# Kernel tuning notes

Measured on AMD Instinct MI355X. Metric: run time of the kernel, lower is better.

The kernel has to match this reference:

```python
import jax, jax.numpy as jnp
import numpy as np

K = 131072
C = 128
THR = 9.2885e-30


def setup_inputs() -> dict:
    key = jax.random.key(0)
    k1, k2, k3, k4, k5 = jax.random.split(key, 5)
    scores1 = jax.random.normal(k1, (K, C), dtype=jnp.float32)
    scores2 = jax.random.normal(k2, (K, C), dtype=jnp.float32)
    # Build lineages hitting the three supported branches, never the
    # unsupported overlapping-but-unequal case (which raises in torch).
    c1 = jax.random.randint(k3, (K,), 0, C)
    off = jax.random.randint(k4, (K,), 1, C)
    c2 = (c1 + off) % C  # guaranteed != c1
    case = jax.random.randint(k5, (K,), 0, 3)  # 0: equal 1-hot, 1: equal 2-hot, 2: disjoint 1-hots
    oh1 = jax.nn.one_hot(c1, C, dtype=jnp.int32)
    oh2 = jax.nn.one_hot(c2, C, dtype=jnp.int32)
    is1 = (case == 1)[:, None]
    is2 = (case == 2)[:, None]
    Y1 = oh1 + jnp.where(is1, oh2, 0)
    Y2 = jnp.where(is2, oh2, Y1)
    return {"scores1": scores1, "Y1": Y1, "scores2": scores2, "Y2": Y2}


def reference(scores1, Y1, scores2, Y2):
    P1 = jax.nn.softmax(scores1, axis=1)  # [K, C]
    P2 = jax.nn.softmax(scores2, axis=1)
    L1 = Y1.astype(P1.dtype)
    L2 = Y2.astype(P2.dtype)

    eq = jnp.all(Y1 == Y2, axis=1)
    s = jnp.sum(Y1, axis=1)
    case1 = eq & (s == 1)   # equal one-hot lineage
    case2 = eq & (s == 2)   # equal two-hot lineage

    nclass = scores1.shape[1]
    rows = jnp.arange(scores1.shape[0])
    idx_a = jnp.argmax(Y1, axis=1)                      # first nonzero
    idx_b = nclass - 1 - jnp.argmax(Y1[:, ::-1], axis=1)  # last nonzero
    p1a = P1[rows, idx_a]; p1b = P1[rows, idx_b]
    p2a = P2[rows, idx_a]; p2b = P2[rows, idx_b]

    def safe_neglog(p):
        return jnp.where(p > THR, -jnp.log(jnp.maximum(p, THR)), 0.0)

    # case1: -log P1[i,c] - log P2[i,c] (each term thresholded)
    loss1 = safe_neglog(p1a) + safe_neglog(p2a)

    # case2: split two-hot into l1 (first pos), l2 (second pos); both one-hot
    # so disjunction == gathered prob.
    prob2 = 1.0 - (1.0 - p1a * p2b) * (1.0 - p1b * p2a)
    loss2 = safe_neglog(prob2)

    # default disjoint case: vectorized disjunction D(l,p) = 1 - prod(1 - l*p)
    D11 = 1.0 - jnp.prod(1.0 - L1 * P1, axis=1)  # Px1_Y1
    D21 = 1.0 - jnp.prod(1.0 - L2 * P1, axis=1)  # Px1_Y2
    D12 = 1.0 - jnp.prod(1.0 - L1 * P2, axis=1)  # Px2_Y1
    D22 = 1.0 - jnp.prod(1.0 - L2 * P2, axis=1)  # Px2_Y2
    probd = 1.0 - (1.0 - D11 * D22) * (1.0 - D21 * D12)
    lossd = safe_neglog(probd)

    return jnp.where(case1, loss1, jnp.where(case2, loss2, lossd))
```

## Files before the change

### kernel.cpp

```cpp
#include <hip/hip_runtime.h>


constexpr int KROWS = 131072;
constexpr int CC    = 128;
#define THRF 9.2885e-30f

typedef float  f32x4 __attribute__((ext_vector_type(4)));
typedef int    i32x4 __attribute__((ext_vector_type(4)));
typedef float  f32x2 __attribute__((ext_vector_type(2)));

__device__ __forceinline__ float hredsumf(float v){
#pragma unroll
  for (int m = 16; m > 0; m >>= 1) v += __shfl_xor(v, m, 32);
  return v;
}

__device__ __forceinline__ float sel4(float p0, float p1, float p2, float p3, int s){
  float lo = (s & 1) ? p1 : p0;
  float hi = (s & 1) ? p3 : p2;
  return (s & 2) ? hi : lo;
}

__device__ __forceinline__ float gatherP(float p0, float p1, float p2, float p3, int idx){
  float c = sel4(p0, p1, p2, p3, idx & 3);
  return __shfl(c, (idx >> 2) & 31, 32);
}

__device__ __forceinline__ float computeRow(
    f32x4 a1, f32x4 a2, i32x4 b1, i32x4 b2, bool hi)
{
  float e10 = __expf(a1.x), e11 = __expf(a1.y), e12 = __expf(a1.z), e13 = __expf(a1.w);
  float e20 = __expf(a2.x), e21 = __expf(a2.y), e22 = __expf(a2.z), e23 = __expf(a2.w);
  float inv1 = 1.0f / hredsumf(e10 + e11 + e12 + e13);
  float inv2 = 1.0f / hredsumf(e20 + e21 + e22 + e23);

  unsigned long long M0 = __ballot((b1.x | b2.x) != 0);
  unsigned long long M1 = __ballot((b1.y | b2.y) != 0);
  unsigned long long M2 = __ballot((b1.z | b2.z) != 0);
  unsigned long long M3 = __ballot((b1.w | b2.w) != 0);

  unsigned int h[4];
  h[0] = hi ? (unsigned int)(M0 >> 32) : (unsigned int)M0;
  h[1] = hi ? (unsigned int)(M1 >> 32) : (unsigned int)M1;
  h[2] = hi ? (unsigned int)(M2 >> 32) : (unsigned int)M2;
  h[3] = hi ? (unsigned int)(M3 >> 32) : (unsigned int)M3;

  int u = 1 << 30, v = -1;
#pragma unroll
  for (int j = 0; j < 4; ++j) {
    if (h[j]) {
      u = min(u, ((__ffs(h[j]) - 1) << 2) + j);
      v = max(v, ((31 - __clz(h[j])) << 2) + j);
    }
  }

  float p1u = gatherP(e10, e11, e12, e13, u) * inv1;
  float p1v = gatherP(e10, e11, e12, e13, v) * inv1;
  float p2u = gatherP(e20, e21, e22, e23, u) * inv2;
  float p2v = gatherP(e20, e21, e22, e23, v) * inv2;

  float x = p1u * p2v;
  float y = p1v * p2u;
  float prob = (u == v) ? x : 1.0f - (1.0f - x) * (1.0f - y);
  return (prob > THRF) ? -__logf(prob) : 0.0f;
}

__global__ __launch_bounds__(256) void wmc_loss_kernel(
    const float* __restrict__ s1, const int* __restrict__ y1,
    const float* __restrict__ s2, const int* __restrict__ y2,
    float* __restrict__ out)
{
  const int hw   = threadIdx.x >> 5;
  const int lane = threadIdx.x & 31;
  const bool hi  = (threadIdx.x & 32) != 0;
  const int row0 = blockIdx.x * 16 + hw * 2;

  const size_t base0 = (size_t)row0 * CC;
  const size_t base1 = base0 + CC;

  const f32x4 A10 = __builtin_nontemporal_load(((const f32x4*)(s1 + base0)) + lane);
  const f32x4 A20 = __builtin_nontemporal_load(((const f32x4*)(s2 + base0)) + lane);
  const i32x4 B10 = __builtin_nontemporal_load(((const i32x4*)(y1 + base0)) + lane);
  const i32x4 B20 = __builtin_nontemporal_load(((const i32x4*)(y2 + base0)) + lane);
  const f32x4 A11 = __builtin_nontemporal_load(((const f32x4*)(s1 + base1)) + lane);
  const f32x4 A21 = __builtin_nontemporal_load(((const f32x4*)(s2 + base1)) + lane);
  const i32x4 B11 = __builtin_nontemporal_load(((const i32x4*)(y1 + base1)) + lane);
  const i32x4 B21 = __builtin_nontemporal_load(((const i32x4*)(y2 + base1)) + lane);

  float l0 = computeRow(A10, A20, B10, B20, hi);
  float l1 = computeRow(A11, A21, B11, B21, hi);

  if (lane == 0) {
    f32x2 o; o.x = l0; o.y = l1;
    __builtin_nontemporal_store(o, (f32x2*)(out + row0));
  }
}

extern "C" void kernel_launch(void* const* d_in, const int* in_sizes, int n_in,
                              void* d_out, int out_size, void* d_ws, size_t ws_size,
                              hipStream_t stream) {
  const float* s1 = (const float*)d_in[0];
  const int*   y1 = (const int*)d_in[1];
  const float* s2 = (const float*)d_in[2];
  const int*   y2 = (const int*)d_in[3];
  float* out = (float*)d_out;

  dim3 grid(KROWS / 16), block(256);
  wmc_loss_kernel<<<grid, block, 0, stream>>>(s1, y1, s2, y2, out);
}
```

Before: 210.1 us.

## Use persistent grid-stride blocks with software-prefetched row pairs

The launch shrinks from one block per 16 rows to 2048 blocks that each loop over 4 row groups. Inside the loop the next iteration's row pair is loaded before the current one is computed. The goal is to overlap global-memory latency with the softmax and gather work and to cut block launch overhead. In exchange each wave holds more live registers for the double-buffered loads, and there are fewer waves in flight to hide latency.

```diff
diff --git a/kernel.cpp b/kernel.cpp
--- a/kernel.cpp
+++ b/kernel.cpp
@@ -1,8 +1,12 @@
 #include <hip/hip_runtime.h>
 
 
-constexpr int KROWS = 131072;
-constexpr int CC    = 128;
+constexpr int KROWS   = 131072;
+constexpr int CC      = 128;
+constexpr int NBLOCKS = 2048;
+constexpr int RPB     = 16;
+constexpr int NITER   = KROWS / (NBLOCKS * RPB);
+constexpr int STRIDE  = NBLOCKS * RPB;
 #define THRF 9.2885e-30f
 
 typedef float  f32x4 __attribute__((ext_vector_type(4)));
@@ -65,6 +69,40 @@
   return (prob > THRF) ? -__logf(prob) : 0.0f;
 }
 
+struct RowPair {
+  f32x4 a10, a20, a11, a21;
+  i32x4 b10, b20, b11, b21;
+};
+
+__device__ __forceinline__ RowPair loadPair(
+    const float* s1, const int* y1, const float* s2, const int* y2,
+    int row0, int lane)
+{
+  RowPair t;
+  const size_t base0 = (size_t)row0 * CC;
+  const size_t base1 = base0 + CC;
+  t.a10 = __builtin_nontemporal_load(((const f32x4*)(s1 + base0)) + lane);
+  t.a20 = __builtin_nontemporal_load(((const f32x4*)(s2 + base0)) + lane);
+  t.b10 = __builtin_nontemporal_load(((const i32x4*)(y1 + base0)) + lane);
+  t.b20 = __builtin_nontemporal_load(((const i32x4*)(y2 + base0)) + lane);
+  t.a11 = __builtin_nontemporal_load(((const f32x4*)(s1 + base1)) + lane);
+  t.a21 = __builtin_nontemporal_load(((const f32x4*)(s2 + base1)) + lane);
+  t.b11 = __builtin_nontemporal_load(((const i32x4*)(y1 + base1)) + lane);
+  t.b21 = __builtin_nontemporal_load(((const i32x4*)(y2 + base1)) + lane);
+  return t;
+}
+
+__device__ __forceinline__ void computeStore(
+    const RowPair& P, bool hi, int lane, int row, float* out)
+{
+  float l0 = computeRow(P.a10, P.a20, P.b10, P.b20, hi);
+  float l1 = computeRow(P.a11, P.a21, P.b11, P.b21, hi);
+  if (lane == 0) {
+    f32x2 o; o.x = l0; o.y = l1;
+    __builtin_nontemporal_store(o, (f32x2*)(out + row));
+  }
+}
+
 __global__ __launch_bounds__(256) void wmc_loss_kernel(
     const float* __restrict__ s1, const int* __restrict__ y1,
     const float* __restrict__ s2, const int* __restrict__ y2,
@@ -73,26 +111,18 @@
   const int hw   = threadIdx.x >> 5;
   const int lane = threadIdx.x & 31;
   const bool hi  = (threadIdx.x & 32) != 0;
-  const int row0 = blockIdx.x * 16 + hw * 2;
+  int row = blockIdx.x * RPB + hw * 2;
 
-  const size_t base0 = (size_t)row0 * CC;
-  const size_t base1 = base0 + CC;
-
-  const f32x4 A10 = __builtin_nontemporal_load(((const f32x4*)(s1 + base0)) + lane);
-  const f32x4 A20 = __builtin_nontemporal_load(((const f32x4*)(s2 + base0)) + lane);
-  const i32x4 B10 = __builtin_nontemporal_load(((const i32x4*)(y1 + base0)) + lane);
-  const i32x4 B20 = __builtin_nontemporal_load(((const i32x4*)(y2 + base0)) + lane);
-  const f32x4 A11 = __builtin_nontemporal_load(((const f32x4*)(s1 + base1)) + lane);
-  const f32x4 A21 = __builtin_nontemporal_load(((const f32x4*)(s2 + base1)) + lane);
-  const i32x4 B11 = __builtin_nontemporal_load(((const i32x4*)(y1 + base1)) + lane);
-  const i32x4 B21 = __builtin_nontemporal_load(((const i32x4*)(y2 + base1)) + lane);
-
-  float l0 = computeRow(A10, A20, B10, B20, hi);
-  float l1 = computeRow(A11, A21, B11, B21, hi);
-
-  if (lane == 0) {
-    f32x2 o; o.x = l0; o.y = l1;
-    __builtin_nontemporal_store(o, (f32x2*)(out + row0));
+  RowPair P = loadPair(s1, y1, s2, y2, row, lane);
+#pragma unroll
+  for (int it = 0; it < NITER; ++it) {
+    const int nrow = row + STRIDE;
+    RowPair N;
+    if (it + 1 < NITER)
+      N = loadPair(s1, y1, s2, y2, nrow, lane);
+    computeStore(P, hi, lane, row, out);
+    P = N;
+    row = nrow;
   }
 }
 
@@ -105,6 +135,6 @@
   const int*   y2 = (const int*)d_in[3];
   float* out = (float*)d_out;
 
-  dim3 grid(KROWS / 16), block(256);
+  dim3 grid(NBLOCKS), block(256);
   wmc_loss_kernel<<<grid, block, 0, stream>>>(s1, y1, s2, y2, out);
 }
```

Measured after the change: 214.6 us. 2.2% more time.
